# Kernel optimization log

Hardware: AMD Instinct MI355X
Metric: run time of the kernel (lower is better)

## Reference

```python
import jax, jax.numpy as jnp
import numpy as np

D_MODEL = 1024
D_STATE = 128
D_CONV = 4
EXPAND = 2
HEADDIM = 64
D_INNER = EXPAND * D_MODEL            # 2048
NHEADS = D_INNER // HEADDIM           # 32
CONV_DIM = D_INNER + 2 * D_STATE      # 2304 (x, B, C share the conv)
D_IN_PROJ = 2 * D_INNER + 2 * D_STATE + NHEADS  # 4384 (z, xBC, dt)
CHUNK = 64
BATCH, SEQ = 8, 2048
EPS = 1e-5


def setup_inputs() -> dict:
    key = jax.random.key(0)
    ks = jax.random.split(key, 8)
    x = jax.random.normal(ks[0], (BATCH, SEQ, D_MODEL), dtype=jnp.float32)
    ln_w = jnp.ones((D_MODEL,), jnp.float32)
    ln_b = jnp.zeros((D_MODEL,), jnp.float32)
    W_in = jax.random.normal(ks[1], (D_IN_PROJ, D_MODEL), jnp.float32) * 0.02
    conv_w = jax.random.normal(ks[2], (CONV_DIM, D_CONV), jnp.float32) * 0.2
    conv_b = jnp.zeros((CONV_DIM,), jnp.float32)
    # dt_bias ~ inverse-softplus of dt in [1e-3, 1e-1]
    dt = jnp.exp(jax.random.uniform(ks[3], (NHEADS,), jnp.float32,
                                    minval=float(np.log(1e-3)), maxval=float(np.log(1e-1))))
    dt_bias = dt + jnp.log(-jnp.expm1(-dt))
    A_log = jnp.log(jax.random.uniform(ks[4], (NHEADS,), jnp.float32, minval=1.0, maxval=16.0))
    D = jnp.ones((NHEADS,), jnp.float32)
    rms_w = jnp.ones((D_INNER,), jnp.float32)
    W_out = jax.random.normal(ks[5], (D_MODEL, D_INNER), jnp.float32) * 0.02
    return {"x": x, "ln_w": ln_w, "ln_b": ln_b, "W_in": W_in, "conv_w": conv_w,
            "conv_b": conv_b, "dt_bias": dt_bias, "A_log": A_log, "D": D,
            "rms_w": rms_w, "W_out": W_out}


def _segsum(a):
    # a: (..., T) -> (..., T, T) cumulative segment sums, -inf above diagonal
    T = a.shape[-1]
    cs = jnp.cumsum(a, axis=-1)
    d = cs[..., :, None] - cs[..., None, :]
    return jnp.where(jnp.tril(jnp.ones((T, T), bool)), d, -jnp.inf)


def _mamba2_layer(x, ln_w, ln_b, W_in, conv_w, conv_b, dt_bias, A_log, D, rms_w, W_out):
    b, l, _ = x.shape
    # LayerNorm
    mu = jnp.mean(x, -1, keepdims=True)
    xc = x - mu
    var = jnp.mean(xc * xc, -1, keepdims=True)
    xn = xc * jax.lax.rsqrt(var + EPS) * ln_w + ln_b
    # in_proj -> z, xBC, dt
    zxbcdt = xn @ W_in.T                                  # (b,l,D_IN_PROJ)
    z = zxbcdt[..., :D_INNER]
    xBC = zxbcdt[..., D_INNER:D_INNER + CONV_DIM]
    dt = zxbcdt[..., D_INNER + CONV_DIM:]
    dt = jax.nn.softplus(dt + dt_bias)                    # (b,l,h)
    # causal depthwise conv1d (kernel D_CONV) + SiLU
    xp = jnp.pad(xBC, ((0, 0), (D_CONV - 1, 0), (0, 0)))
    conv = conv_b + sum(xp[:, k:k + l, :] * conv_w[:, k] for k in range(D_CONV))
    xBC = conv * jax.nn.sigmoid(conv)
    xs = xBC[..., :D_INNER].reshape(b, l, NHEADS, HEADDIM)          # (b,l,h,p)
    Bm = xBC[..., D_INNER:D_INNER + D_STATE]                         # (b,l,n) ngroups=1
    Cm = xBC[..., D_INNER + D_STATE:]                                # (b,l,n)
    # SSD chunked scan
    A = -jnp.exp(A_log)                                              # (h,)
    A_dt = dt * A                                                    # (b,l,h)
    Xdt = xs * dt[..., None]                                         # (b,l,h,p)
    nc = l // CHUNK
    Xc = Xdt.reshape(b, nc, CHUNK, NHEADS, HEADDIM)                  # (b,c,s,h,p)
    Ac = A_dt.reshape(b, nc, CHUNK, NHEADS).transpose(0, 3, 1, 2)    # (b,h,c,s)
    Bc = Bm.reshape(b, nc, CHUNK, D_STATE)                           # (b,c,s,n)
    Cc = Cm.reshape(b, nc, CHUNK, D_STATE)
    A_cs = jnp.cumsum(Ac, -1)                                        # (b,h,c,s)
    Lmat = jnp.exp(_segsum(Ac))                                      # (b,h,c,s,s)
    Y_diag = jnp.einsum('bcln,bcsn,bhcls,bcshp->bclhp', Cc, Bc, Lmat, Xc)
    decay_states = jnp.exp(A_cs[..., -1:] - A_cs)                    # (b,h,c,s)
    states = jnp.einsum('bcln,bhcl,bclhp->bchpn', Bc, decay_states, Xc)
    states = jnp.concatenate([jnp.zeros_like(states[:, :1]), states], axis=1)
    chunk_sum = jnp.pad(A_cs[..., -1], ((0, 0), (0, 0), (1, 0)))     # (b,h,c+1)
    decay_chunk = jnp.exp(_segsum(chunk_sum))                        # (b,h,c+1,c+1)
    new_states = jnp.einsum('bhzc,bchpn->bzhpn', decay_chunk, states)
    states_prev = new_states[:, :-1]                                 # (b,c,h,p,n)
    state_decay_out = jnp.exp(A_cs)                                  # (b,h,c,s)
    Y_off = jnp.einsum('bcln,bchpn,bhcl->bclhp', Cc, states_prev, state_decay_out)
    Y = (Y_diag + Y_off).reshape(b, l, NHEADS, HEADDIM)
    Y = Y + xs * D[None, None, :, None]
    y = Y.reshape(b, l, D_INNER)
    # gated RMSNorm: gate first, then normalize
    y = y * (z * jax.nn.sigmoid(z))
    y = y * jax.lax.rsqrt(jnp.mean(y * y, -1, keepdims=True) + EPS) * rms_w
    out = y @ W_out.T
    return x + out


def reference(x, ln_w, ln_b, W_in, conv_w, conv_b, dt_bias, A_log, D, rms_w, W_out):
    return _mamba2_layer(x, ln_w, ln_b, W_in, conv_w, conv_b, dt_bias, A_log, D, rms_w, W_out)
```

## Files before the change

kernel.cpp:

```cpp
#include <hip/hip_runtime.h>
#include <hip/hip_bf16.h>
#include <math.h>

typedef __hip_bfloat16 bf16;
typedef short short8 __attribute__((ext_vector_type(8)));
typedef short short4v __attribute__((ext_vector_type(4)));
typedef float f32x4 __attribute__((ext_vector_type(4)));

#define B_ 8
#define L_ 2048
#define DM 1024
#define DI 2048
#define NH 32
#define HD 64
#define DS 128
#define NWPAD 4608
#define XW 2432
#define CONVD 2304
#define NC 32
#define CK 64
#define HG 16
#define NGRP (NH / HG)
#define BL (B_ * L_)

static __device__ __forceinline__ f32x4 mfma_bf16(short8 a, short8 b, f32x4 c) {
  asm("v_mfma_f32_16x16x32_bf16 %0, %1, %2, %0" : "+v"(c) : "v"(a), "v"(b));
  return c;
}

static __device__ __forceinline__ void gload16(const bf16* g, bf16* l) {
  __builtin_amdgcn_global_load_lds((const __attribute__((address_space(1))) void*)g,
                                   (__attribute__((address_space(3))) void*)l, 16, 0, 0);
}

static __device__ __forceinline__ short bf2s(float f) {
  bf16 b = __float2bfloat16(f);
  return *reinterpret_cast<short*>(&b);
}

static __device__ __forceinline__ float s2f(short s) {
  unsigned int u = ((unsigned int)(unsigned short)s) << 16;
  return __uint_as_float(u);
}

__global__ void cvt_k(const float* __restrict__ Wi, const float* __restrict__ Wo,
                      bf16* __restrict__ Wib, bf16* __restrict__ Wob) {
  size_t i = (size_t)blockIdx.x * 256 + threadIdx.x;
  const size_t NWI = (size_t)NWPAD * DM;
  if (i < NWI) {
    float v = (i < (size_t)4384 * 1024) ? Wi[i] : 0.f;
    Wib[i] = __float2bfloat16(v);
  } else {
    size_t j = i - NWI;
    Wob[j] = __float2bfloat16(Wo[j]);
  }
}

__global__ void ln_k(const float* __restrict__ x, const float* __restrict__ w,
                     const float* __restrict__ bz, bf16* __restrict__ xn) {
  __shared__ float sm1[4], sm2[4];
  int row = blockIdx.x, tid = threadIdx.x;
  int d0 = tid * 4;
  const float* xr = x + (size_t)row * DM;
  float4 v4 = *(const float4*)&xr[d0];
  float v[4] = {v4.x, v4.y, v4.z, v4.w};
  float s = v[0] + v[1] + v[2] + v[3];
#pragma unroll
  for (int o = 32; o > 0; o >>= 1) s += __shfl_down(s, o, 64);
  if ((tid & 63) == 0) sm1[tid >> 6] = s;
  __syncthreads();
  float mean = (sm1[0] + sm1[1] + sm1[2] + sm1[3]) * (1.f / DM);
  float q = 0.f;
#pragma unroll
  for (int i = 0; i < 4; i++) { float d = v[i] - mean; q += d * d; }
#pragma unroll
  for (int o = 32; o > 0; o >>= 1) q += __shfl_down(q, o, 64);
  if ((tid & 63) == 0) sm2[tid >> 6] = q;
  __syncthreads();
  float rstd = rsqrtf((sm2[0] + sm2[1] + sm2[2] + sm2[3]) * (1.f / DM) + 1e-5f);
  float4 w4 = *(const float4*)&w[d0];
  float4 b4 = *(const float4*)&bz[d0];
  short4v o4;
  o4[0] = bf2s((v[0] - mean) * rstd * w4.x + b4.x);
  o4[1] = bf2s((v[1] - mean) * rstd * w4.y + b4.y);
  o4[2] = bf2s((v[2] - mean) * rstd * w4.z + b4.z);
  o4[3] = bf2s((v[3] - mean) * rstd * w4.w + b4.w);
  *(short4v*)&xn[(size_t)row * DM + d0] = o4;
}

static __device__ __forceinline__ void stage_half(const bf16* __restrict__ gbase, int Kd,
                                                  bf16* lbase, int H, int kti,
                                                  int srow, int schunk, int wave) {
  int gc = (schunk ^ (srow & 7)) << 3;
  const bf16* g = gbase + (size_t)(H * 128 + srow) * Kd + (size_t)kti * 64 + gc;
  bf16* l = lbase + (H * 128 + wave * 8) * 64;
  gload16(g, l);
  gload16(g + (size_t)64 * Kd, l + 64 * 64);
}

#define BARM asm volatile("s_barrier" ::: "memory")

#define RD_A(mi)                                                                \
  {                                                                             \
    int r = wm + (mi) * 16 + (lane & 15);                                       \
    int k0 = lane >> 4;                                                         \
    af[mi][0] = *(const short8*)&Asb[r * 64 + ((k0 ^ (r & 7)) << 3)];           \
    af[mi][1] = *(const short8*)&Asb[r * 64 + (((k0 + 4) ^ (r & 7)) << 3)];     \
  }
#define RD_B(ni)                                                                \
  {                                                                             \
    int r = wn + (ni) * 16 + (lane & 15);                                       \
    int k0 = lane >> 4;                                                         \
    bfr[ni][0] = *(const short8*)&Bsb[r * 64 + ((k0 ^ (r & 7)) << 3)];          \
    bfr[ni][1] = *(const short8*)&Bsb[r * 64 + (((k0 + 4) ^ (r & 7)) << 3)];    \
  }
#define MFMA_Q(q)                                                               \
  __builtin_amdgcn_s_setprio(1);                                                \
  _Pragma("unroll") for (int ni = 0; ni < 4; ni++)                              \
    acc[2*(q)][ni] = mfma_bf16(af[2*(q)][0], bfr[ni][0], acc[2*(q)][ni]);       \
  _Pragma("unroll") for (int ni = 0; ni < 4; ni++)                              \
    acc[2*(q)+1][ni] = mfma_bf16(af[2*(q)+1][0], bfr[ni][0], acc[2*(q)+1][ni]); \
  _Pragma("unroll") for (int ni = 0; ni < 4; ni++)                              \
    acc[2*(q)][ni] = mfma_bf16(af[2*(q)][1], bfr[ni][1], acc[2*(q)][ni]);       \
  _Pragma("unroll") for (int ni = 0; ni < 4; ni++)                              \
    acc[2*(q)+1][ni] = mfma_bf16(af[2*(q)+1][1], bfr[ni][1], acc[2*(q)+1][ni]); \
  __builtin_amdgcn_s_setprio(0);

#define TILE4(b, t, Kd)                                                         \
  {                                                                             \
    const bf16* Asb = &As[b][0];                                                \
    const bf16* Bsb = &Bs[b][0];                                                \
    const int i1 = ((t) + 1 < NKT) ? (t) + 1 : NKT - 1;                         \
    const int i2 = ((t) + 2 < NKT) ? (t) + 2 : NKT - 1;                         \
    RD_B(0) RD_B(1) RD_B(2) RD_B(3)                                             \
    RD_A(0) RD_A(1)                                                             \
    stage_half(Ag, Kd, &As[(b) ^ 1][0], 1, i1, srow, schunk, wave);             \
    asm volatile("s_waitcnt lgkmcnt(8)" ::: "memory");                          \
    BARM;                                                                       \
    MFMA_Q(0)                                                                   \
    BARM;                                                                       \
    RD_A(2) RD_A(3) RD_A(4) RD_A(5)                                             \
    stage_half(Bg, Kd, &Bs[b][0], 0, i2, srow, schunk, wave);                   \
    BARM;                                                                       \
    MFMA_Q(1)                                                                   \
    BARM;                                                                       \
    RD_A(6) RD_A(7)                                                             \
    stage_half(Bg, Kd, &Bs[b][0], 1, i2, srow, schunk, wave);                   \
    asm volatile("s_waitcnt lgkmcnt(0)" ::: "memory");                          \
    BARM;                                                                       \
    MFMA_Q(2)                                                                   \
    BARM;                                                                       \
    stage_half(Ag, Kd, &As[b][0], 0, i2, srow, schunk, wave);                   \
    asm volatile("s_waitcnt vmcnt(6)" ::: "memory");                            \
    BARM;                                                                       \
    MFMA_Q(3)                                                                   \
    BARM;                                                                       \
  }

#define GEMM8_BODY(Kd)                                                          \
  const int tid = threadIdx.x;                                                  \
  const int lane = tid & 63;                                                    \
  const int wave = tid >> 6;                                                    \
  int nwg = gridDim.x * gridDim.y;                                              \
  int id = blockIdx.y * gridDim.x + blockIdx.x;                                 \
  int bx = blockIdx.x, by = blockIdx.y;                                         \
  if ((nwg & 7) == 0) {                                                         \
    int swz = (id & 7) * (nwg >> 3) + (id >> 3);                                \
    bx = swz % gridDim.x;                                                       \
    by = swz / gridDim.x;                                                       \
  }                                                                             \
  const int m0 = by * 256, n0 = bx * 256;                                       \
  const int wm = (wave >> 2) * 128, wn = (wave & 3) * 64;                       \
  const int srow = tid >> 3, schunk = tid & 7;                                  \
  const bf16* Ag = A + (size_t)m0 * (Kd);                                       \
  const bf16* Bg = Bw + (size_t)n0 * (Kd);                                      \
  const int NKT = (Kd) / 64;                                                    \
  f32x4 acc[8][4];                                                              \
  short8 af[8][2], bfr[4][2];                                                   \
  _Pragma("unroll") for (int i = 0; i < 8; i++)                                 \
    _Pragma("unroll") for (int j = 0; j < 4; j++)                               \
      acc[i][j] = (f32x4){0.f, 0.f, 0.f, 0.f};                                  \
  stage_half(Bg, Kd, &Bs[0][0], 0, 0, srow, schunk, wave);                      \
  stage_half(Bg, Kd, &Bs[0][0], 1, 0, srow, schunk, wave);                      \
  stage_half(Ag, Kd, &As[0][0], 0, 0, srow, schunk, wave);                      \
  stage_half(Ag, Kd, &As[0][0], 1, 0, srow, schunk, wave);                      \
  asm volatile("s_waitcnt vmcnt(4)" ::: "memory");                              \
  stage_half(Bg, Kd, &Bs[1][0], 0, 1, srow, schunk, wave);                      \
  stage_half(Bg, Kd, &Bs[1][0], 1, 1, srow, schunk, wave);                      \
  stage_half(Ag, Kd, &As[1][0], 0, 1, srow, schunk, wave);                      \
  asm volatile("s_waitcnt vmcnt(6)" ::: "memory");                              \
  BARM;                                                                         \
  for (int t = 0; t < NKT; t += 2) {                                            \
    TILE4(0, t, Kd)                                                             \
    TILE4(1, t + 1, Kd)                                                         \
  }                                                                             \
  asm volatile("s_waitcnt vmcnt(0)" ::: "memory");                              \
  asm volatile("s_nop 7\n\ts_nop 7" ::);                                        \
  const int orow = (lane >> 4) << 2;                                            \
  const int ocol = lane & 15;

__global__ __launch_bounds__(512, 2) void gemm_inproj_k(
    const bf16* __restrict__ A, const bf16* __restrict__ Bw,
    bf16* __restrict__ zb, bf16* __restrict__ xb) {
  __shared__ bf16 As[2][256 * 64];
  __shared__ bf16 Bs[2][256 * 64];
  GEMM8_BODY(DM)
#pragma unroll
  for (int mi = 0; mi < 8; mi++) {
#pragma unroll
    for (int ni = 0; ni < 4; ni++) {
      int rbase = m0 + wm + mi * 16 + orow;
      int cc = n0 + wn + ni * 16 + ocol;
#pragma unroll
      for (int r = 0; r < 4; r++) {
        bf16 v = __float2bfloat16(acc[mi][ni][r]);
        if (cc < DI)               zb[(size_t)(rbase + r) * DI + cc] = v;
        else if (cc < DI + XW)     xb[(size_t)(rbase + r) * XW + (cc - DI)] = v;
      }
    }
  }
}

__global__ __launch_bounds__(512, 2) void gemm_out_k(
    const bf16* __restrict__ A, const bf16* __restrict__ Bw,
    float* __restrict__ C, const float* __restrict__ resid) {
  __shared__ bf16 As[2][256 * 64];
  __shared__ bf16 Bs[2][256 * 64];
  GEMM8_BODY(DI)
#pragma unroll
  for (int mi = 0; mi < 8; mi++) {
#pragma unroll
    for (int ni = 0; ni < 4; ni++) {
      int rbase = m0 + wm + mi * 16 + orow;
      int cc = n0 + wn + ni * 16 + ocol;
#pragma unroll
      for (int r = 0; r < 4; r++) {
        size_t idx = (size_t)(rbase + r) * DM + cc;
        C[idx] = acc[mi][ni][r] + resid[idx];
      }
    }
  }
}

__global__ void conv_k(const bf16* __restrict__ xbc, const float* __restrict__ conv_w,
                       const float* __restrict__ conv_b, bf16* __restrict__ xsb,
                       bf16* __restrict__ Bb, bf16* __restrict__ Cb) {
  int c = blockIdx.x * 256 + threadIdx.x;
  int lbase = blockIdx.y * 16;
  int b = blockIdx.z;
  float4 w = ((const float4*)conv_w)[c];
  float bias = conv_b[c];
  const bf16* xp = xbc + (size_t)b * L_ * XW + c;
  float h0 = 0.f, h1 = 0.f, h2 = 0.f;
  if (lbase > 0) {
    h0 = __bfloat162float(xp[(size_t)(lbase - 3) * XW]);
    h1 = __bfloat162float(xp[(size_t)(lbase - 2) * XW]);
    h2 = __bfloat162float(xp[(size_t)(lbase - 1) * XW]);
  }
  for (int t = 0; t < 16; t++) {
    int l = lbase + t;
    float x3 = __bfloat162float(xp[(size_t)l * XW]);
    float v = bias + w.x * h0 + w.y * h1 + w.z * h2 + w.w * x3;
    v = v / (1.f + __expf(-v));
    bf16 o = __float2bfloat16(v);
    size_t rl = (size_t)b * L_ + l;
    if (c < DI)           xsb[rl * DI + c] = o;
    else if (c < DI + DS) Bb[rl * DS + (c - DI)] = o;
    else                  Cb[rl * DS + (c - DI - DS)] = o;
    h0 = h1; h1 = h2; h2 = x3;
  }
}

__global__ void dt_k(const bf16* __restrict__ xbc, const float* __restrict__ dt_bias,
                     const float* __restrict__ A_log, float* __restrict__ dtsp,
                     float* __restrict__ dta) {
  size_t i = (size_t)blockIdx.x * 256 + threadIdx.x;
  int h = (int)(i >> 14);
  size_t row = i & 16383;
  float raw = __bfloat162float(xbc[row * XW + CONVD + h]) + dt_bias[h];
  float sp = (raw > 20.f) ? raw : log1pf(__expf(raw));
  dtsp[i] = sp;
  dta[i] = -__expf(A_log[h]) * sp;
}

__global__ __launch_bounds__(256) void chunk_g_k(
    const bf16* __restrict__ xsb, const bf16* __restrict__ Bb, const bf16* __restrict__ Cb,
    const float* __restrict__ dtsp, const float* __restrict__ dta,
    const float* __restrict__ Dv, int hbase,
    bf16* __restrict__ Y, bf16* __restrict__ states, float* __restrict__ cs63) {
  __shared__ __align__(16) bf16 Bs[64][136];
  __shared__ __align__(16) bf16 Cs[64][136];
  __shared__ __align__(16) bf16 Btw[128][72];
  __shared__ __align__(16) bf16 Xt[64][72];
  __shared__ __align__(16) bf16 Sb[64][72];
  __shared__ float cs[64];
  __shared__ float wts[64];
  __shared__ float dts[64];

  int hgsub = blockIdx.x, c = blockIdx.y, b = blockIdx.z;
  int tid = threadIdx.x;
  int lane = tid & 63, wid = tid >> 6;
  size_t l0 = (size_t)b * L_ + (size_t)c * CK;

  for (int i = tid; i < 64 * 16; i += 256) {
    int r = i >> 4, n8 = (i & 15) << 3;
    *(short8*)&Bs[r][n8] = *(const short8*)&Bb[(l0 + r) * DS + n8];
    *(short8*)&Cs[r][n8] = *(const short8*)&Cb[(l0 + r) * DS + n8];
  }
  __syncthreads();

  f32x4 accg[4];
#pragma unroll
  for (int i = 0; i < 4; i++) accg[i] = (f32x4){0.f, 0.f, 0.f, 0.f};
  {
    int rb = wid * 16 + (lane & 15);
    int c0 = (lane >> 4) * 8;
#pragma unroll
    for (int kk = 0; kk < 4; kk++) {
      int kc = c0 + kk * 32;
      short8 bfrag = *(const short8*)&Bs[rb][kc];
#pragma unroll
      for (int lt = 0; lt < 4; lt++) {
        short8 afrag = *(const short8*)&Cs[lt * 16 + (lane & 15)][kc];
        accg[lt] = mfma_bf16(afrag, bfrag, accg[lt]);
      }
    }
  }
  asm volatile("s_nop 7\n\ts_nop 7" ::);

  for (int hh = 0; hh < 8; hh++) {
    int hl = hgsub * 8 + hh;
    int h = hbase + hl;
    __syncthreads();

    {
      const bf16* xp = xsb + l0 * DI + h * HD + lane;
      for (int oct = wid; oct < 8; oct += 4) {
        int lb = oct * 8;
        short8 v;
#pragma unroll
        for (int j = 0; j < 8; j++)
          v[j] = *(const short*)&xp[(size_t)(lb + j) * DI];
        *(short8*)&Xt[lane][lb] = v;
      }
    }
    if (tid < 64) {
      dts[tid] = dtsp[(size_t)h * BL + l0 + tid];
      wts[tid] = dta[(size_t)h * BL + l0 + tid];
    }
    __syncthreads();
    if (tid < 64) {
      float a = wts[tid];
#pragma unroll
      for (int o = 1; o < 64; o <<= 1) {
        float t = __shfl_up(a, o, 64);
        if (lane >= o) a += t;
      }
      cs[tid] = a;
      float tot = __shfl(a, 63, 64);
      if (tid == 63) cs63[((size_t)b * NH + h) * NC + c] = a;
      wts[tid] = __expf(tot - a) * dts[tid];
    }
    __syncthreads();

    for (int u = wid; u < 16; u += 4) {
      int nh = u & 1, oct = u >> 1;
      int n = nh * 64 + lane;
      int lb = oct * 8;
      short8 v;
#pragma unroll
      for (int j = 0; j < 8; j++)
        v[j] = bf2s(__bfloat162float(Bs[lb + j][n]) * wts[lb + j]);
      *(short8*)&Btw[n][lb] = v;
    }
    {
      int s = wid * 16 + (lane & 15);
      float css = cs[s], dtss = dts[s];
#pragma unroll
      for (int lt = 0; lt < 4; lt++) {
#pragma unroll
        for (int r = 0; r < 4; r++) {
          int l = lt * 16 + ((lane >> 4) << 2) + r;
          float v = (s <= l) ? accg[lt][r] * __expf(cs[l] - css) * dtss : 0.f;
          Sb[l][s] = __float2bfloat16(v);
        }
      }
    }
    __syncthreads();

    f32x4 accy[4];
#pragma unroll
    for (int i = 0; i < 4; i++) accy[i] = (f32x4){0.f, 0.f, 0.f, 0.f};
    {
      int prow = wid * 16 + (lane & 15);
      int c0 = (lane >> 4) * 8;
#pragma unroll
      for (int kk = 0; kk < 2; kk++) {
        int kc = c0 + kk * 32;
        short8 xfrag = *(const short8*)&Xt[prow][kc];
#pragma unroll
        for (int lt = 0; lt < 4; lt++) {
          short8 sfrag = *(const short8*)&Sb[lt * 16 + (lane & 15)][kc];
          accy[lt] = mfma_bf16(sfrag, xfrag, accy[lt]);
        }
      }
    }
    f32x4 accs[4][2];
#pragma unroll
    for (int i = 0; i < 4; i++)
#pragma unroll
      for (int j = 0; j < 2; j++) accs[i][j] = (f32x4){0.f, 0.f, 0.f, 0.f};
    {
      int c0 = (lane >> 4) * 8;
#pragma unroll
      for (int kk = 0; kk < 2; kk++) {
        int kc = c0 + kk * 32;
        short8 bf0 = *(const short8*)&Btw[wid * 32 + (lane & 15)][kc];
        short8 bf1 = *(const short8*)&Btw[wid * 32 + 16 + (lane & 15)][kc];
#pragma unroll
        for (int pt = 0; pt < 4; pt++) {
          short8 xfrag = *(const short8*)&Xt[pt * 16 + (lane & 15)][kc];
          accs[pt][0] = mfma_bf16(xfrag, bf0, accs[pt][0]);
          accs[pt][1] = mfma_bf16(xfrag, bf1, accs[pt][1]);
        }
      }
    }
    asm volatile("s_nop 7\n\ts_nop 7" ::);
    {
      float Dh = Dv[h];
      int p = wid * 16 + (lane & 15);
#pragma unroll
      for (int lt = 0; lt < 4; lt++) {
#pragma unroll
        for (int r = 0; r < 4; r++) {
          int l = lt * 16 + ((lane >> 4) << 2) + r;
          float xv = __bfloat162float(Xt[p][l]);
          Y[(l0 + l) * DI + h * HD + p] = __float2bfloat16(accy[lt][r] + Dh * xv);
        }
      }
    }
    {
      size_t sbb = ((((size_t)b * NC + c) * HG + hl) * HD) * DS;
#pragma unroll
      for (int pt = 0; pt < 4; pt++)
#pragma unroll
        for (int tn = 0; tn < 2; tn++)
#pragma unroll
          for (int r = 0; r < 4; r++) {
            int p = pt * 16 + ((lane >> 4) << 2) + r;
            int n = wid * 32 + tn * 16 + (lane & 15);
            states[sbb + (size_t)p * DS + n] = __float2bfloat16(accs[pt][tn][r]);
          }
    }
  }
}

__global__ void scan_k(bf16* __restrict__ states, const float* __restrict__ cs63,
                       int hbase) {
  int hl = blockIdx.x, b = blockIdx.y, sp = blockIdx.z;
  int tid = threadIdx.x;
  const float* csb = cs63 + ((size_t)b * NH + hbase + hl) * NC;
  int e0 = sp * 1024 + tid * 4;
  float S0 = 0.f, S1 = 0.f, S2 = 0.f, S3 = 0.f;
  for (int c = 0; c < NC; c++) {
    bf16* p = states + ((((size_t)b * NC + c) * HG + hl) * HD) * DS + e0;
    float d = __expf(csb[c]);
    short4v cur = *(const short4v*)p;
    short4v prev;
    prev[0] = bf2s(S0); prev[1] = bf2s(S1); prev[2] = bf2s(S2); prev[3] = bf2s(S3);
    *(short4v*)p = prev;
    S0 = S0 * d + s2f(cur[0]);
    S1 = S1 * d + s2f(cur[1]);
    S2 = S2 * d + s2f(cur[2]);
    S3 = S3 * d + s2f(cur[3]);
  }
}

__global__ __launch_bounds__(256) void yoff_k(
    const bf16* __restrict__ Cb, const bf16* __restrict__ states,
    const float* __restrict__ dta, int hbase, bf16* __restrict__ Y) {
  __shared__ __align__(16) bf16 Cs[64][136];
  __shared__ __align__(16) bf16 Sp[64][136];
  __shared__ float cs[64];
  int hl = blockIdx.x, c = blockIdx.y, b = blockIdx.z;
  int h = hbase + hl;
  int tid = threadIdx.x;
  int lane = tid & 63, wid = tid >> 6;
  size_t l0 = (size_t)b * L_ + (size_t)c * CK;
  for (int i = tid; i < 64 * 16; i += 256) {
    int r = i >> 4, n8 = (i & 15) << 3;
    *(short8*)&Cs[r][n8] = *(const short8*)&Cb[(l0 + r) * DS + n8];
  }
  size_t sbb = ((((size_t)b * NC + c) * HG + hl) * HD) * DS;
  for (int i = tid; i < 64 * 16; i += 256) {
    int p = i >> 4, n8 = (i & 15) << 3;
    *(short8*)&Sp[p][n8] = *(const short8*)&states[sbb + (size_t)p * DS + n8];
  }
  if (tid < 64) cs[tid] = dta[(size_t)h * BL + l0 + tid];
  __syncthreads();
  if (tid < 64) {
    float a = cs[tid];
#pragma unroll
    for (int o = 1; o < 64; o <<= 1) {
      float t = __shfl_up(a, o, 64);
      if (lane >= o) a += t;
    }
    cs[tid] = a;
  }
  __syncthreads();
  f32x4 acc[4];
#pragma unroll
  for (int i = 0; i < 4; i++) acc[i] = (f32x4){0.f, 0.f, 0.f, 0.f};
  {
    int prow = wid * 16 + (lane & 15);
    int c0 = (lane >> 4) * 8;
#pragma unroll
    for (int kk = 0; kk < 4; kk++) {
      int kc = c0 + kk * 32;
      short8 sfrag = *(const short8*)&Sp[prow][kc];
#pragma unroll
      for (int lt = 0; lt < 4; lt++) {
        short8 cfrag = *(const short8*)&Cs[lt * 16 + (lane & 15)][kc];
        acc[lt] = mfma_bf16(cfrag, sfrag, acc[lt]);
      }
    }
  }
  asm volatile("s_nop 7\n\ts_nop 7" ::);
  {
    int p = wid * 16 + (lane & 15);
#pragma unroll
    for (int lt = 0; lt < 4; lt++) {
#pragma unroll
      for (int r = 0; r < 4; r++) {
        int l = lt * 16 + ((lane >> 4) << 2) + r;
        float e = __expf(cs[l]);
        size_t idx = (l0 + l) * DI + h * HD + p;
        Y[idx] = __float2bfloat16(__bfloat162float(Y[idx]) + e * acc[lt][r]);
      }
    }
  }
}

__global__ void gate_k(const bf16* __restrict__ Y, const bf16* __restrict__ z,
                       const float* __restrict__ rms_w, bf16* __restrict__ yb) {
  __shared__ float sm[4];
  int row = blockIdx.x, tid = threadIdx.x;
  int d0 = tid * 8;
  const bf16* Yr = Y + (size_t)row * DI;
  const bf16* zr = z + (size_t)row * DI;
  short8 yv8 = *(const short8*)&Yr[d0];
  short8 zv8 = *(const short8*)&zr[d0];
  float v[8]; float ss = 0.f;
#pragma unroll
  for (int i = 0; i < 8; i++) {
    float yv = s2f(yv8[i]);
    float zz = s2f(zv8[i]);
    yv *= zz / (1.f + __expf(-zz));
    v[i] = yv; ss += yv * yv;
  }
#pragma unroll
  for (int o = 32; o > 0; o >>= 1) ss += __shfl_down(ss, o, 64);
  if ((tid & 63) == 0) sm[tid >> 6] = ss;
  __syncthreads();
  float rstd = rsqrtf((sm[0] + sm[1] + sm[2] + sm[3]) * (1.f / DI) + 1e-5f);
  short8 o8;
#pragma unroll
  for (int i = 0; i < 8; i++) o8[i] = bf2s(v[i] * rstd * rms_w[d0 + i]);
  *(short8*)&yb[(size_t)row * DI + d0] = o8;
}

extern "C" void kernel_launch(void* const* d_in, const int* in_sizes, int n_in,
                              void* d_out, int out_size, void* d_ws, size_t ws_size,
                              hipStream_t stream) {
  const float* x       = (const float*)d_in[0];
  const float* ln_w    = (const float*)d_in[1];
  const float* ln_b    = (const float*)d_in[2];
  const float* W_in    = (const float*)d_in[3];
  const float* conv_w  = (const float*)d_in[4];
  const float* conv_b  = (const float*)d_in[5];
  const float* dt_bias = (const float*)d_in[6];
  const float* A_log   = (const float*)d_in[7];
  const float* Dv      = (const float*)d_in[8];
  const float* rms_w   = (const float*)d_in[9];
  const float* W_out   = (const float*)d_in[10];
  float* out = (float*)d_out;

  char* ws = (char*)d_ws;
  size_t off = 0;
  auto alloc = [&](size_t bytes) -> void* {
    void* p = ws + off;
    off += (bytes + 255) & ~(size_t)255;
    return p;
  };
  bf16*  W_in_b  = (bf16*)alloc((size_t)NWPAD * DM * 2);
  bf16*  W_out_b = (bf16*)alloc((size_t)DM * DI * 2);
  bf16*  R1      = (bf16*)alloc((size_t)BL * XW * 2);
  bf16*  R2      = (bf16*)alloc((size_t)BL * DI * 2);
  bf16*  Bb      = (bf16*)alloc((size_t)BL * DS * 2);
  bf16*  Cb      = (bf16*)alloc((size_t)BL * DS * 2);
  float* dtsp    = (float*)alloc((size_t)BL * NH * 4);
  float* dta     = (float*)alloc((size_t)BL * NH * 4);
  float* cs63    = (float*)alloc((size_t)B_ * NH * NC * 4);
  bf16* xbcdt  = R1;
  bf16* states = R1;
  bf16* yb     = R1;
  bf16* xn     = R2;
  bf16* xsb    = R2;
  bf16* zbuf   = (bf16*)d_out;
  (void)ws_size; (void)in_sizes; (void)n_in; (void)out_size;

  cvt_k <<<(NWPAD * DM + DM * DI) / 256, 256, 0, stream>>>(W_in, W_out, W_in_b, W_out_b);
  ln_k  <<<BL, 256, 0, stream>>>(x, ln_w, ln_b, xn);
  gemm_inproj_k<<<dim3(NWPAD / 256, BL / 256), 512, 0, stream>>>(
      xn, W_in_b, zbuf, xbcdt);
  conv_k<<<dim3(CONVD / 256, L_ / 16, B_), 256, 0, stream>>>(
      xbcdt, conv_w, conv_b, xsb, Bb, Cb);
  dt_k  <<<(BL * NH) / 256, 256, 0, stream>>>(xbcdt, dt_bias, A_log, dtsp, dta);
  for (int g = 0; g < NGRP; g++) {
    int hbase = g * HG;
    chunk_g_k<<<dim3(2, NC, B_), 256, 0, stream>>>(xsb, Bb, Cb, dtsp, dta, Dv, hbase,
                                                   xsb , states, cs63);
    scan_k   <<<dim3(HG, B_, 8), 256, 0, stream>>>(states, cs63, hbase);
    yoff_k   <<<dim3(HG, NC, B_), 256, 0, stream>>>(Cb, states, dta, hbase, xsb );
  }
  gate_k<<<BL, 256, 0, stream>>>(xsb , zbuf, rms_w, yb);
  gemm_out_k<<<dim3(DM / 256, BL / 256), 512, 0, stream>>>(yb, W_out_b, out, x);
}
```

Baseline: 567.7 us.

## Replace in-proj GEMM with simple 128x128 tile kernel and trim weight padding

The in-projection GEMM moves from the 256x256 double-buffered, hand-pipelined 8-wave kernel to a plain 128x128 single-buffer kernel with 4 waves, and the padded weight width drops from 4608 to 4480. The aim is to cut wasted padded columns and get better tile quantization across CUs. The cost is no global-to-LDS overlap and lower per-block reuse. The out-projection pipeline also switches to builtin barriers with sched_barrier fences and changes one lgkmcnt wait from 8 to 4.

New measurement: 570.7 us. No clear change (+0.5%).

```diff
diff --git a/kernel.cpp b/kernel.cpp
--- a/kernel.cpp
+++ b/kernel.cpp
@@ -14,7 +14,7 @@
 #define NH 32
 #define HD 64
 #define DS 128
-#define NWPAD 4608
+#define NWPAD 4480
 #define XW 2432
 #define CONVD 2304
 #define NC 32
@@ -88,6 +88,89 @@
   *(short4v*)&xn[(size_t)row * DM + d0] = o4;
 }
 
+#define GEMM_PROLOGUE(Kdim)                                                     \
+  const int tid = threadIdx.x;                                                  \
+  const int lane = tid & 63;                                                    \
+  const int wave = tid >> 6;                                                    \
+  int nwg = gridDim.x * gridDim.y;                                              \
+  int id = blockIdx.y * gridDim.x + blockIdx.x;                                 \
+  int bx = blockIdx.x, by = blockIdx.y;                                         \
+  if ((nwg & 7) == 0) {                                                         \
+    int swz = (id & 7) * (nwg >> 3) + (id >> 3);                                \
+    bx = swz % gridDim.x;                                                       \
+    by = swz / gridDim.x;                                                       \
+  }                                                                             \
+  const int m0 = by * 128, n0 = bx * 128;                                       \
+  const int wm = (wave >> 1) * 64, wn = (wave & 1) * 64;                        \
+  const int srow = tid >> 3;                                                    \
+  const int schunk = tid & 7;                                                   \
+  f32x4 acc[4][4];                                                              \
+  _Pragma("unroll")                                                             \
+  for (int i = 0; i < 4; i++)                                                   \
+    _Pragma("unroll")                                                           \
+    for (int j = 0; j < 4; j++) acc[i][j] = (f32x4){0.f, 0.f, 0.f, 0.f};        \
+  for (int kt = 0; kt < (Kdim); kt += 64) {                                     \
+    __syncthreads();                                                            \
+    _Pragma("unroll")                                                           \
+    for (int is = 0; is < 4; is++) {                                            \
+      int row = is * 32 + srow;                                                 \
+      int gcol = (schunk ^ (row & 7)) << 3;                                     \
+      const bf16* ga = A + (size_t)(m0 + row) * (Kdim) + kt + gcol;             \
+      const bf16* gb = Bw + (size_t)(n0 + row) * (Kdim) + kt + gcol;            \
+      bf16* la = &As[(is * 32 + wave * 8) * 64];                                \
+      bf16* lb = &Bs[(is * 32 + wave * 8) * 64];                                \
+      gload16(ga, la);                                                          \
+      gload16(gb, lb);                                                          \
+    }                                                                           \
+    __syncthreads();                                                            \
+    _Pragma("unroll")                                                           \
+    for (int kk = 0; kk < 2; kk++) {                                            \
+      short8 af[4], bfr[4];                                                     \
+      int mrow = lane & 15;                                                     \
+      int kch = kk * 4 + (lane >> 4);                                           \
+      _Pragma("unroll")                                                         \
+      for (int mi = 0; mi < 4; mi++) {                                          \
+        int r = wm + mi * 16 + mrow;                                            \
+        af[mi] = *(const short8*)&As[r * 64 + ((kch ^ (r & 7)) << 3)];          \
+      }                                                                         \
+      _Pragma("unroll")                                                         \
+      for (int ni = 0; ni < 4; ni++) {                                          \
+        int r = wn + ni * 16 + mrow;                                            \
+        bfr[ni] = *(const short8*)&Bs[r * 64 + ((kch ^ (r & 7)) << 3)];         \
+      }                                                                         \
+      _Pragma("unroll")                                                         \
+      for (int mi = 0; mi < 4; mi++)                                            \
+        _Pragma("unroll")                                                       \
+        for (int ni = 0; ni < 4; ni++)                                          \
+          acc[mi][ni] = mfma_bf16(af[mi], bfr[ni], acc[mi][ni]);                \
+    }                                                                           \
+  }                                                                             \
+  asm volatile("s_nop 7\n\ts_nop 7" ::);                                        \
+  const int orow = (lane >> 4) << 2;                                            \
+  const int ocol = lane & 15;
+
+__global__ __launch_bounds__(256) void gemm_inproj_k(
+    const bf16* __restrict__ A, const bf16* __restrict__ Bw,
+    bf16* __restrict__ zb, bf16* __restrict__ xb) {
+  __shared__ bf16 As[128 * 64];
+  __shared__ bf16 Bs[128 * 64];
+  GEMM_PROLOGUE(DM)
+#pragma unroll
+  for (int mi = 0; mi < 4; mi++) {
+#pragma unroll
+    for (int ni = 0; ni < 4; ni++) {
+      int rbase = m0 + wm + mi * 16 + orow;
+      int cc = n0 + wn + ni * 16 + ocol;
+#pragma unroll
+      for (int r = 0; r < 4; r++) {
+        bf16 v = __float2bfloat16(acc[mi][ni][r]);
+        if (cc < DI) zb[(size_t)(rbase + r) * DI + cc] = v;
+        else         xb[(size_t)(rbase + r) * XW + (cc - DI)] = v;
+      }
+    }
+  }
+}
+
 static __device__ __forceinline__ void stage_half(const bf16* __restrict__ gbase, int Kd,
                                                   bf16* lbase, int H, int kti,
                                                   int srow, int schunk, int wave) {
@@ -98,7 +181,13 @@
   gload16(g + (size_t)64 * Kd, l + 64 * 64);
 }
 
-#define BARM asm volatile("s_barrier" ::: "memory")
+#define SYNC __builtin_amdgcn_s_barrier()
+#define WAIT_LGKM(n)                                                            \
+  asm volatile("s_waitcnt lgkmcnt(" #n ")" ::: "memory");                       \
+  __builtin_amdgcn_sched_barrier(0)
+#define WAIT_VM(n)                                                              \
+  asm volatile("s_waitcnt vmcnt(" #n ")" ::: "memory");                         \
+  __builtin_amdgcn_sched_barrier(0)
 
 #define RD_A(mi)                                                                \
   {                                                                             \
@@ -135,26 +224,26 @@
     RD_B(0) RD_B(1) RD_B(2) RD_B(3)                                             \
     RD_A(0) RD_A(1)                                                             \
     stage_half(Ag, Kd, &As[(b) ^ 1][0], 1, i1, srow, schunk, wave);             \
-    asm volatile("s_waitcnt lgkmcnt(8)" ::: "memory");                          \
-    BARM;                                                                       \
+    WAIT_LGKM(4);                      \
+    SYNC;                                                                       \
     MFMA_Q(0)                                                                   \
-    BARM;                                                                       \
+    SYNC;                                                                       \
     RD_A(2) RD_A(3) RD_A(4) RD_A(5)                                             \
     stage_half(Bg, Kd, &Bs[b][0], 0, i2, srow, schunk, wave);                   \
-    BARM;                                                                       \
+    SYNC;                                                                       \
     MFMA_Q(1)                                                                   \
-    BARM;                                                                       \
+    SYNC;                                                                       \
     RD_A(6) RD_A(7)                                                             \
     stage_half(Bg, Kd, &Bs[b][0], 1, i2, srow, schunk, wave);                   \
-    asm volatile("s_waitcnt lgkmcnt(0)" ::: "memory");                          \
-    BARM;                                                                       \
+    WAIT_LGKM(0);                                      \
+    SYNC;                                                                       \
     MFMA_Q(2)                                                                   \
-    BARM;                                                                       \
+    SYNC;                                                                       \
     stage_half(Ag, Kd, &As[b][0], 0, i2, srow, schunk, wave);                   \
-    asm volatile("s_waitcnt vmcnt(6)" ::: "memory");                            \
-    BARM;                                                                       \
+    WAIT_VM(6);                                 \
+    SYNC;                                                                       \
     MFMA_Q(3)                                                                   \
-    BARM;                                                                       \
+    SYNC;                                                                       \
   }
 
 #define GEMM8_BODY(Kd)                                                          \
@@ -184,42 +273,20 @@
   stage_half(Bg, Kd, &Bs[0][0], 1, 0, srow, schunk, wave);                      \
   stage_half(Ag, Kd, &As[0][0], 0, 0, srow, schunk, wave);                      \
   stage_half(Ag, Kd, &As[0][0], 1, 0, srow, schunk, wave);                      \
-  asm volatile("s_waitcnt vmcnt(4)" ::: "memory");                              \
+  WAIT_VM(4);                                                                   \
   stage_half(Bg, Kd, &Bs[1][0], 0, 1, srow, schunk, wave);                      \
   stage_half(Bg, Kd, &Bs[1][0], 1, 1, srow, schunk, wave);                      \
   stage_half(Ag, Kd, &As[1][0], 0, 1, srow, schunk, wave);                      \
-  asm volatile("s_waitcnt vmcnt(6)" ::: "memory");                              \
-  BARM;                                                                         \
+  WAIT_VM(6);                                                                   \
+  SYNC;                                                                         \
   for (int t = 0; t < NKT; t += 2) {                                            \
     TILE4(0, t, Kd)                                                             \
     TILE4(1, t + 1, Kd)                                                         \
   }                                                                             \
-  asm volatile("s_waitcnt vmcnt(0)" ::: "memory");                              \
+  WAIT_VM(0);                                                                   \
   asm volatile("s_nop 7\n\ts_nop 7" ::);                                        \
   const int orow = (lane >> 4) << 2;                                            \
   const int ocol = lane & 15;
-
-__global__ __launch_bounds__(512, 2) void gemm_inproj_k(
-    const bf16* __restrict__ A, const bf16* __restrict__ Bw,
-    bf16* __restrict__ zb, bf16* __restrict__ xb) {
-  __shared__ bf16 As[2][256 * 64];
-  __shared__ bf16 Bs[2][256 * 64];
-  GEMM8_BODY(DM)
-#pragma unroll
-  for (int mi = 0; mi < 8; mi++) {
-#pragma unroll
-    for (int ni = 0; ni < 4; ni++) {
-      int rbase = m0 + wm + mi * 16 + orow;
-      int cc = n0 + wn + ni * 16 + ocol;
-#pragma unroll
-      for (int r = 0; r < 4; r++) {
-        bf16 v = __float2bfloat16(acc[mi][ni][r]);
-        if (cc < DI)               zb[(size_t)(rbase + r) * DI + cc] = v;
-        else if (cc < DI + XW)     xb[(size_t)(rbase + r) * XW + (cc - DI)] = v;
-      }
-    }
-  }
-}
 
 __global__ __launch_bounds__(512, 2) void gemm_out_k(
     const bf16* __restrict__ A, const bf16* __restrict__ Bw,
@@ -611,7 +678,7 @@
 
   cvt_k <<<(NWPAD * DM + DM * DI) / 256, 256, 0, stream>>>(W_in, W_out, W_in_b, W_out_b);
   ln_k  <<<BL, 256, 0, stream>>>(x, ln_w, ln_b, xn);
-  gemm_inproj_k<<<dim3(NWPAD / 256, BL / 256), 512, 0, stream>>>(
+  gemm_inproj_k<<<dim3(NWPAD / 128, BL / 128), 256, 0, stream>>>(
       xn, W_in_b, zbuf, xbcdt);
   conv_k<<<dim3(CONVD / 256, L_ / 16, B_), 256, 0, stream>>>(
       xbcdt, conv_w, conv_b, xsb, Bb, Cb);
```
